# Kernel optimization log

Measured on AMD Instinct MI355X. Metric: run time of the kernel, lower is better.

## Reference

```python
import jax, jax.numpy as jnp
import numpy as np

# Module config (defaults from __init__) and attention sizing
T, H, W = 16, 32, 32          # resolution (t, h, w)
KT, KS = 7, 7                 # window_size_t, window_size_s (dilation = 1)
HEADS, HEAD_DIM = 8, 64
C = HEADS * HEAD_DIM          # 512
B = 1                         # true batch; hidden_states leading dim = B*H*W


def nb_idx(L, K):
    """NATTEN (dilation=1) neighborhood indices: window of size K centered at i,
    shifted (clamped) at borders so it always stays in-bounds. -> [L, K] int."""
    i = jnp.arange(L)
    start = jnp.clip(i - K // 2, 0, L - K)
    return start[:, None] + jnp.arange(K)[None, :]


def setup_inputs() -> dict:
    key = jax.random.key(0)
    ks = jax.random.split(key, 5)
    x = jax.random.normal(ks[0], (B * H * W, T, C), jnp.float32)
    w_q = jax.random.normal(ks[1], (C, C), jnp.float32) * 0.02
    w_k = jax.random.normal(ks[2], (C, C), jnp.float32) * 0.02
    w_v = jax.random.normal(ks[3], (C, C), jnp.float32) * 0.02
    w_o = jax.random.normal(ks[4], (C, C), jnp.float32) * 0.02
    b_o = jnp.zeros((C,), jnp.float32)
    return {"hidden_states": x, "w_q": w_q, "w_k": w_k, "w_v": w_v,
            "w_o": w_o, "b_o": b_o}


def _attend(q, k, v):
    """3D neighborhood attention (natten3dqk + softmax + natten3dav).
    q, k, v: [b, nh, T, H, W, hd] fp32 -> out: [b, nh, T, H, W, hd].
    Scans over the KT*KS*KS = 343 window offsets so only one shifted copy of
    k / v is materialized at a time (faithful to NATTEN's locally-sparse math)."""
    t_nb, h_nb, w_nb = nb_idx(T, KT), nb_idx(H, KS), nb_idx(W, KS)
    g = jnp.meshgrid(jnp.arange(KT), jnp.arange(KS), jnp.arange(KS), indexing='ij')
    offs = tuple(a.reshape(-1) for a in g)

    def gather(x, j):
        jt, jh, jw = j
        kt, kh, kw = t_nb[:, jt], h_nb[:, jh], w_nb[:, jw]  # [T],[H],[W]
        return x[:, :, kt[:, None, None], kh[None, :, None], kw[None, None, :], :]

    @jax.checkpoint
    def qk_step(_, j):
        # raw dot product, no scaling (matches the explicit natten3dqk call)
        return None, jnp.einsum('bnthwd,bnthwd->bnthw', q, gather(k, j))

    _, qk = jax.lax.scan(qk_step, None, offs)          # [343, b, nh, T, H, W]
    ats = jax.nn.softmax(qk, axis=0)                   # softmax over neighbors

    @jax.checkpoint
    def av_step(acc, inp):
        j, a = inp                                     # a: [b, nh, T, H, W]
        return acc + a[..., None] * gather(v, j), None

    out, _ = jax.lax.scan(av_step, jnp.zeros_like(q), (offs, ats))
    return out


def reference(hidden_states, w_q, w_k, w_v, w_o, b_o):
    bhw, t, c = hidden_states.shape                    # [(b h w), T, C]
    b = bhw // (H * W)

    q = hidden_states @ w_q
    k = hidden_states @ w_k
    v = hidden_states @ w_v

    def to_heads(x):  # '(b h w) t (nh hd) -> b nh t h w hd'
        x = x.reshape(b, H, W, T, HEADS, HEAD_DIM)
        return jnp.transpose(x, (0, 4, 3, 1, 2, 5))

    q, k, v = (to_heads(x).astype(jnp.float32) for x in (q, k, v))

    out = _attend(q, k, v)                             # [b, nh, T, H, W, hd]

    # 'b nh t h w hd -> (b h w) t (nh hd)'
    out = jnp.transpose(out, (0, 3, 4, 2, 1, 5)).reshape(bhw, T, C)
    return out @ w_o + b_o                             # to_out[0]; dropout = id
```

## Files before the change

kernel.cpp:

```cpp
#include <hip/hip_runtime.h>

typedef unsigned int u32;
typedef unsigned short u16;
typedef __attribute__((ext_vector_type(8))) __bf16 bf16x8;
typedef __attribute__((ext_vector_type(4))) float f32x4;
typedef __attribute__((ext_vector_type(2))) unsigned int u32x2;

#define T_   16
#define HH   32
#define WW   32
#define HEADS_ 8
#define HD_  64
#define CC   512
#define NPOS 16384
#define QKS  1024

__device__ __forceinline__ u16 f2bf(float f){
  u32 u = __builtin_bit_cast(u32, f);
  u32 r = u + 0x7FFFu + ((u >> 16) & 1u);
  return (u16)(r >> 16);
}

__device__ __forceinline__ u32 cvt_pk_bf16(float lo, float hi){
  u32 r;
  asm("v_cvt_pk_bf16_f32 %0, %1, %2" : "=v"(r) : "v"(lo), "v"(hi));
  return r;
}

__device__ __forceinline__ void gload16(const void* g, void* l){
  __builtin_amdgcn_global_load_lds(
    (const __attribute__((address_space(1))) void*)g,
    (__attribute__((address_space(3))) void*)l, 16, 0, 0);
}

__global__ __launch_bounds__(256) void k_convert_x(const float* __restrict__ x,
                                                   u16* __restrict__ xb){
  int i = blockIdx.x * 256 + threadIdx.x;
  const float4 a = ((const float4*)x)[i*2];
  const float4 b = ((const float4*)x)[i*2+1];
  union { u16 h[8]; uint4 q; } o;
  o.h[0]=f2bf(a.x); o.h[1]=f2bf(a.y); o.h[2]=f2bf(a.z); o.h[3]=f2bf(a.w);
  o.h[4]=f2bf(b.x); o.h[5]=f2bf(b.y); o.h[6]=f2bf(b.z); o.h[7]=f2bf(b.w);
  ((uint4*)xb)[i] = o.q;
}

__global__ __launch_bounds__(256) void k_convert_w(const float* __restrict__ wq,
                                                   const float* __restrict__ wk,
                                                   const float* __restrict__ wv,
                                                   const float* __restrict__ wo,
                                                   u16* __restrict__ wt,
                                                   u16* __restrict__ wot){
  int i = blockIdx.x * 256 + threadIdx.x;
  if (i < 1536*512){
    int n = i >> 9, k = i & 511;
    const float* src = (n < 512) ? wq : (n < 1024) ? wk : wv;
    wt[i] = f2bf(src[k*512 + (n & 511)]);
  } else {
    int j = i - 1536*512;
    int n = j >> 9, k = j & 511;
    wot[j] = f2bf(wo[k*512 + n]);
  }
}

template<int OUTMODE>
__global__ __launch_bounds__(256) void k_gemm_bt(
    const u16* __restrict__ A, const u16* __restrict__ Bt,
    void* __restrict__ C, const float* __restrict__ bias,
    int M, int N, int K)
{
  __shared__ u16 lds[2][2][128*32];
  const int tid = threadIdx.x;
  const int lane = tid & 63;
  const int l15 = lane & 15, lhi = lane >> 4;
  const int wv = tid >> 6;
  const int gx = gridDim.x;
  const int nwg = gx * gridDim.y;
  int flat = blockIdx.y * gx + blockIdx.x;
  flat = (flat & 7) * (nwg >> 3) + (flat >> 3);
  const int tm = (flat / gx) * 128, tn = (flat % gx) * 128;
  const int wm = (wv >> 1) * 64, wn = (wv & 1) * 64;
  const int nk = K >> 5;

  auto stage = [&](int buf, int kb){
    #pragma unroll
    for (int half = 0; half < 2; ++half){
      int c = tid + half*256;
      int row = c >> 2;
      int g = (c & 3) ^ ((c >> 3) & 3);
      char* la = (char*)(&lds[buf][0][0]) + ((c >> 6) << 10);
      gload16(A + (size_t)(tm + row) * K + (kb << 5) + (g << 3), la);
      char* lb = (char*)(&lds[buf][1][0]) + ((c >> 6) << 10);
      gload16(Bt + (size_t)(tn + row) * K + (kb << 5) + (g << 3), lb);
    }
  };

  stage(0, 0);
  f32x4 acc[4][4];
  const f32x4 z4 = {0.f, 0.f, 0.f, 0.f};
  #pragma unroll
  for (int i = 0; i < 4; ++i)
    #pragma unroll
    for (int j = 0; j < 4; ++j) acc[i][j] = z4;
  __syncthreads();

  int buf = 0;
  for (int kb = 0; kb < nk; ++kb){
    if (kb + 1 < nk) stage(buf ^ 1, kb + 1);
    const char* la = (const char*)(&lds[buf][0][0]);
    const char* lb = (const char*)(&lds[buf][1][0]);
    bf16x8 af[4], bfr[4];
    #pragma unroll
    for (int ai = 0; ai < 4; ++ai){
      int row = wm + ai*16 + l15;
      af[ai] = *(const bf16x8*)(la + row*64 + ((lhi ^ ((row >> 1) & 3)) << 4));
    }
    #pragma unroll
    for (int bj = 0; bj < 4; ++bj){
      int row = wn + bj*16 + l15;
      bfr[bj] = *(const bf16x8*)(lb + row*64 + ((lhi ^ ((row >> 1) & 3)) << 4));
    }
    #pragma unroll
    for (int ai = 0; ai < 4; ++ai)
      #pragma unroll
      for (int bj = 0; bj < 4; ++bj)
        acc[ai][bj] = __builtin_amdgcn_mfma_f32_16x16x32_bf16(af[ai], bfr[bj], acc[ai][bj], 0, 0, 0);
    __syncthreads();
    buf ^= 1;
  }

  #pragma unroll
  for (int ai = 0; ai < 4; ++ai)
    #pragma unroll
    for (int bj = 0; bj < 4; ++bj)
      #pragma unroll
      for (int r = 0; r < 4; ++r){
        int rr = tm + wm + ai*16 + (lhi << 2) + r;
        int cc = tn + wn + bj*16 + l15;
        float v = acc[ai][bj][r];
        if (OUTMODE == 0) ((u16*)C)[(size_t)rr * N + cc] = f2bf(v);
        else              ((float*)C)[(size_t)rr * N + cc] = v + bias[cc];
      }
}

__global__ __launch_bounds__(512) void k_attn(const u16* __restrict__ qkv,
                                              const u16* __restrict__ vt,
                                              u16* __restrict__ ao){
  __shared__ u16 ldsK[2][16384];
  __shared__ u16 ldsV[2][16384];
  const int tid = threadIdx.x;
  const int lane = tid & 63;
  const int wv = tid >> 6;
  const int l15 = lane & 15, lhi = lane >> 4;
  const int bid = blockIdx.x;
  const int head = bid & 7;
  const int sp = bid >> 3;
  const int hrow = sp >> 2, wg = sp & 3;
  const int wq = (wg << 3) + wv;
  const int hw = (hrow << 5) + wq;
  const int hs = min(max(hrow - 3, 0), HH - 7);
  const int cb = min(max((wg << 3) - 3, 0), 18);
  const int offw = min(max(wq - 3, 0), WW - 7) - cb;

  const size_t qoff = ((size_t)hw * 16 + l15) * QKS + head * HD_ + (lhi << 3);
  const bf16x8 qb0 = *(const bf16x8*)(qkv + qoff);
  const bf16x8 qb1 = *(const bf16x8*)(qkv + qoff + 32);

  const int tst = min(max(l15 - 3, 0), T_ - 7);
  bool val[4];
  #pragma unroll
  for (int r = 0; r < 4; ++r){
    int tp = (lhi << 2) + r;
    val[r] = (tp >= tst) && (tp < tst + 7);
  }

  const int srcb = l15 + ((lhi & 1) << 5);
  const bool bval = (lhi < 2);

  auto stageK = [&](int buf, int jh){
    const int hw0 = ((hs + jh) << 5) + cb;
    #pragma unroll
    for (int rnd = 0; rnd < 4; ++rnd){
      int c = tid + (rnd << 9);
      int lc = c ^ ((c >> 3) & 7);
      int s = lc >> 7, tt = (lc >> 3) & 15, ch16 = lc & 7;
      const u16* src = qkv + ((size_t)(hw0 + s) * 16 + tt) * QKS + CC + head * HD_ + (ch16 << 3);
      gload16(src, &ldsK[buf][(size_t)((rnd << 9) + (wv << 6)) * 8]);
    }
  };
  auto stageV = [&](int buf, int jh){
    const int mb = (((hs + jh) << 5) + cb) << 4;
    #pragma unroll
    for (int rnd = 0; rnd < 4; ++rnd){
      int c = tid + (rnd << 9);
      int lc = c ^ ((c >> 5) & 7);
      int d = lc >> 5, m16 = lc & 31;
      const u16* src = vt + (((size_t)(head * HD_ + d)) << 14) + mb + (m16 << 3);
      gload16(src, &ldsV[buf][(size_t)((rnd << 9) + (wv << 6)) * 8]);
    }
  };

  float mrun = -3.0e38f, lp = 0.f;
  f32x4 oacc[4];
  const f32x4 z4 = {0.f,0.f,0.f,0.f};
  #pragma unroll
  for (int c = 0; c < 4; ++c) oacc[c] = z4;

  stageK(0, 0); stageV(0, 0);
  __syncthreads();

  int buf = 0;
  const int sw_ = (l15 & 7) << 4;
  for (int jh = 0; jh < 7; ++jh){
    if (jh < 6){ stageK(buf ^ 1, jh + 1); stageV(buf ^ 1, jh + 1); }
    const char* KB = (const char*)&ldsK[buf][0];
    const char* VB = (const char*)&ldsV[buf][0];

    f32x4 st[7];
    #pragma unroll
    for (int s = 0; s < 7; ++s){
      const int ab = ((offw + s) << 11) + (l15 << 7) + (lhi << 4);
      const bf16x8 ka0 = *(const bf16x8*)(KB + ((ab)      ^ sw_));
      const bf16x8 ka1 = *(const bf16x8*)(KB + ((ab + 64) ^ sw_));
      f32x4 acc = z4;
      acc = __builtin_amdgcn_mfma_f32_16x16x32_bf16(ka0, qb0, acc, 0, 0, 0);
      acc = __builtin_amdgcn_mfma_f32_16x16x32_bf16(ka1, qb1, acc, 0, 0, 0);
      st[s] = acc;
    }
    float tmax = -3.0e38f;
    #pragma unroll
    for (int s = 0; s < 7; ++s)
      #pragma unroll
      for (int r = 0; r < 4; ++r){
        float sv = val[r] ? st[s][r] : -1.0e30f;
        st[s][r] = sv;
        tmax = fmaxf(tmax, sv);
      }
    tmax = fmaxf(tmax, __shfl_xor(tmax, 16));
    tmax = fmaxf(tmax, __shfl_xor(tmax, 32));
    const float mnew = fmaxf(mrun, tmax);
    const float sc = __expf(mrun - mnew);
    mrun = mnew;
    lp *= sc;
    #pragma unroll
    for (int c = 0; c < 4; ++c){
      oacc[c][0] *= sc; oacc[c][1] *= sc; oacc[c][2] *= sc; oacc[c][3] *= sc;
    }
    #pragma unroll
    for (int s = 0; s < 7; ++s){
      float p0 = __expf(st[s][0] - mnew);
      float p1 = __expf(st[s][1] - mnew);
      float p2 = __expf(st[s][2] - mnew);
      float p3 = __expf(st[s][3] - mnew);
      lp += (p0 + p1) + (p2 + p3);
      u32 px = cvt_pk_bf16(p0, p1);
      u32 py = cvt_pk_bf16(p2, p3);
      u32 w0 = __shfl(px, srcb);
      u32 w1 = __shfl(py, srcb);
      u32 w2 = __shfl(px, srcb + 16);
      u32 w3 = __shfl(py, srcb + 16);
      union { u32 u[4]; bf16x8 v; } bb;
      bb.u[0] = bval ? w0 : 0u;
      bb.u[1] = bval ? w1 : 0u;
      bb.u[2] = bval ? w2 : 0u;
      bb.u[3] = bval ? w3 : 0u;
      #pragma unroll
      for (int c = 0; c < 4; ++c){
        const int d = (c << 4) + l15;
        const int vb_ = (d << 9) + ((offw + s) << 5) + (lhi << 4);
        const bf16x8 va = *(const bf16x8*)(VB + (vb_ ^ sw_));
        oacc[c] = __builtin_amdgcn_mfma_f32_16x16x32_bf16(va, bb.v, oacc[c], 0, 0, 0);
      }
    }
    __syncthreads();
    buf ^= 1;
  }

  float lsum = lp;
  lsum += __shfl_xor(lsum, 16);
  lsum += __shfl_xor(lsum, 32);
  const float inv = 1.0f / lsum;

  const size_t obase = ((size_t)hw * 16 + l15) * CC + head * HD_ + (lhi << 2);
  #pragma unroll
  for (int c = 0; c < 4; ++c){
    u32x2 o;
    o.x = cvt_pk_bf16(oacc[c][0] * inv, oacc[c][1] * inv);
    o.y = cvt_pk_bf16(oacc[c][2] * inv, oacc[c][3] * inv);
    *(u32x2*)(ao + obase + c * 16) = o;
  }
}

extern "C" void kernel_launch(void* const* d_in, const int* in_sizes, int n_in,
                              void* d_out, int out_size, void* d_ws, size_t ws_size,
                              hipStream_t stream){
  const float* x  = (const float*)d_in[0];
  const float* wq = (const float*)d_in[1];
  const float* wk = (const float*)d_in[2];
  const float* wv = (const float*)d_in[3];
  const float* wo = (const float*)d_in[4];
  const float* bo = (const float*)d_in[5];

  char* ws = (char*)d_ws;
  u16* Xb  = (u16*)(ws);
  u16* Wt  = (u16*)(ws + 16777216);
  u16* Wot = (u16*)(ws + 18350080);
  u16* QKV = (u16*)(ws + 18874368);
  u16* Vt  = (u16*)(ws + 52428800);
  u16* AO  = (u16*)(ws + 69206016);

  k_convert_x<<<4096, 256, 0, stream>>>(x, Xb);
  k_convert_w<<<4096, 256, 0, stream>>>(wq, wk, wv, wo, Wt, Wot);
  { dim3 g(8, 128);  k_gemm_bt<0><<<g, 256, 0, stream>>>(Xb, Wt, QKV, nullptr, 16384, 1024, 512); }
  { dim3 g(128, 4);  k_gemm_bt<0><<<g, 256, 0, stream>>>(Wt + 1024*512, Xb, Vt, nullptr, 512, 16384, 512); }
  k_attn<<<1024, 512, 0, stream>>>(QKV, Vt, AO);
  { dim3 g(4, 128);  k_gemm_bt<1><<<g, 256, 0, stream>>>(AO, Wot, (float*)d_out, bo, 16384, 512, 512); }
}
```

Measured before the change: 158.7 us.

## Software-pipeline QK and PV across window rows; fold log2e into Wq for exp2

Restructures the neighborhood-attention loop so the QK MFMAs for row jh are issued together with the PV MFMAs of row jh-1, with K staged one row ahead and V staged one row behind. The bf16 probabilities are kept in registers between iterations. The intent is to overlap softmax and exp latency with matrix work. Separately, Wq is pre-scaled by log2(e) so the softmax can use exp2f directly. This raises register pressure and slightly alters rounding, since the scaled weights are rounded to bf16.

```diff
diff --git a/kernel.cpp b/kernel.cpp
--- a/kernel.cpp
+++ b/kernel.cpp
@@ -54,7 +54,8 @@
   if (i < 1536*512){
     int n = i >> 9, k = i & 511;
     const float* src = (n < 512) ? wq : (n < 1024) ? wk : wv;
-    wt[i] = f2bf(src[k*512 + (n & 511)]);
+    float scl = (n < 512) ? 1.44269504088896f : 1.0f;
+    wt[i] = f2bf(src[k*512 + (n & 511)] * scl);
   } else {
     int j = i - 1536*512;
     int n = j >> 9, k = j & 511;
@@ -199,23 +200,16 @@
     }
   };
 
+  const int sw_ = (l15 & 7) << 4;
+  const f32x4 z4 = {0.f,0.f,0.f,0.f};
+
   float mrun = -3.0e38f, lp = 0.f;
   f32x4 oacc[4];
-  const f32x4 z4 = {0.f,0.f,0.f,0.f};
   #pragma unroll
   for (int c = 0; c < 4; ++c) oacc[c] = z4;
-
-  stageK(0, 0); stageV(0, 0);
-  __syncthreads();
-
-  int buf = 0;
-  const int sw_ = (l15 & 7) << 4;
-  for (int jh = 0; jh < 7; ++jh){
-    if (jh < 6){ stageK(buf ^ 1, jh + 1); stageV(buf ^ 1, jh + 1); }
-    const char* KB = (const char*)&ldsK[buf][0];
-    const char* VB = (const char*)&ldsV[buf][0];
-
-    f32x4 st[7];
+  u32 bb7[7][4];
+
+  auto qk = [&](const char* KB, f32x4 (&st)[7]){
     #pragma unroll
     for (int s = 0; s < 7; ++s){
       const int ab = ((offw + s) << 11) + (l15 << 7) + (lhi << 4);
@@ -226,6 +220,23 @@
       acc = __builtin_amdgcn_mfma_f32_16x16x32_bf16(ka1, qb1, acc, 0, 0, 0);
       st[s] = acc;
     }
+  };
+  auto pv = [&](const char* VB){
+    #pragma unroll
+    for (int s = 0; s < 7; ++s){
+      union { u32 u[4]; bf16x8 v; } bb;
+      bb.u[0] = bb7[s][0]; bb.u[1] = bb7[s][1];
+      bb.u[2] = bb7[s][2]; bb.u[3] = bb7[s][3];
+      #pragma unroll
+      for (int c = 0; c < 4; ++c){
+        const int d = (c << 4) + l15;
+        const int vb_ = (d << 9) + ((offw + s) << 5) + (lhi << 4);
+        const bf16x8 va = *(const bf16x8*)(VB + (vb_ ^ sw_));
+        oacc[c] = __builtin_amdgcn_mfma_f32_16x16x32_bf16(va, bb.v, oacc[c], 0, 0, 0);
+      }
+    }
+  };
+  auto softmax_pack = [&](f32x4 (&st)[7]) -> float {
     float tmax = -3.0e38f;
     #pragma unroll
     for (int s = 0; s < 7; ++s)
@@ -238,19 +249,15 @@
     tmax = fmaxf(tmax, __shfl_xor(tmax, 16));
     tmax = fmaxf(tmax, __shfl_xor(tmax, 32));
     const float mnew = fmaxf(mrun, tmax);
-    const float sc = __expf(mrun - mnew);
+    const float sc = exp2f(mrun - mnew);
     mrun = mnew;
     lp *= sc;
     #pragma unroll
-    for (int c = 0; c < 4; ++c){
-      oacc[c][0] *= sc; oacc[c][1] *= sc; oacc[c][2] *= sc; oacc[c][3] *= sc;
-    }
-    #pragma unroll
     for (int s = 0; s < 7; ++s){
-      float p0 = __expf(st[s][0] - mnew);
-      float p1 = __expf(st[s][1] - mnew);
-      float p2 = __expf(st[s][2] - mnew);
-      float p3 = __expf(st[s][3] - mnew);
+      float p0 = exp2f(st[s][0] - mnew);
+      float p1 = exp2f(st[s][1] - mnew);
+      float p2 = exp2f(st[s][2] - mnew);
+      float p3 = exp2f(st[s][3] - mnew);
       lp += (p0 + p1) + (p2 + p3);
       u32 px = cvt_pk_bf16(p0, p1);
       u32 py = cvt_pk_bf16(p2, p3);
@@ -258,22 +265,46 @@
       u32 w1 = __shfl(py, srcb);
       u32 w2 = __shfl(px, srcb + 16);
       u32 w3 = __shfl(py, srcb + 16);
-      union { u32 u[4]; bf16x8 v; } bb;
-      bb.u[0] = bval ? w0 : 0u;
-      bb.u[1] = bval ? w1 : 0u;
-      bb.u[2] = bval ? w2 : 0u;
-      bb.u[3] = bval ? w3 : 0u;
-      #pragma unroll
-      for (int c = 0; c < 4; ++c){
-        const int d = (c << 4) + l15;
-        const int vb_ = (d << 9) + ((offw + s) << 5) + (lhi << 4);
-        const bf16x8 va = *(const bf16x8*)(VB + (vb_ ^ sw_));
-        oacc[c] = __builtin_amdgcn_mfma_f32_16x16x32_bf16(va, bb.v, oacc[c], 0, 0, 0);
-      }
+      bb7[s][0] = bval ? w0 : 0u;
+      bb7[s][1] = bval ? w1 : 0u;
+      bb7[s][2] = bval ? w2 : 0u;
+      bb7[s][3] = bval ? w3 : 0u;
+    }
+    return sc;
+  };
+
+  stageK(0, 0);
+  __syncthreads();
+
+  {
+    stageK(1, 1);
+    stageV(0, 0);
+    f32x4 st[7];
+    qk((const char*)&ldsK[0][0], st);
+    const float sc = softmax_pack(st);
+    #pragma unroll
+    for (int c = 0; c < 4; ++c){
+      oacc[c][0] *= sc; oacc[c][1] *= sc; oacc[c][2] *= sc; oacc[c][3] *= sc;
     }
     __syncthreads();
-    buf ^= 1;
-  }
+  }
+
+  for (int jh = 1; jh < 7; ++jh){
+    const int buf = jh & 1;
+    if (jh < 6) stageK(buf ^ 1, jh + 1);
+    stageV(buf, jh);
+    f32x4 st[7];
+    qk((const char*)&ldsK[buf][0], st);
+    pv((const char*)&ldsV[buf ^ 1][0]);
+    const float sc = softmax_pack(st);
+    #pragma unroll
+    for (int c = 0; c < 4; ++c){
+      oacc[c][0] *= sc; oacc[c][1] *= sc; oacc[c][2] *= sc; oacc[c][3] *= sc;
+    }
+    __syncthreads();
+  }
+
+  pv((const char*)&ldsV[0][0]);
 
   float lsum = lp;
   lsum += __shfl_xor(lsum, 16);
```

After: 171.4 us. +8.0%, slower.
